# Performance work log

Hardware: AMD Instinct MI355X
Metric: run time of the kernel (lower is better)

## Reference

```python
import jax, jax.numpy as jnp
import numpy as np

B, K, N = 8, 4, 131072
DENSITY = 0.3
NEG_PAD = -1000.0
NEG_IDLE = -1.0e8


def setup_inputs() -> dict:
    rng = np.random.default_rng(0)
    mask_s = rng.random((B, K, N)) < DENSITY  # bool, per-slot variable counts
    mask_a = rng.random((B, K, N)) < DENSITY
    ts = int(mask_s.sum())
    ta = int(mask_a.sum())
    key = jax.random.key(0)
    k1, k2, k3, k4 = jax.random.split(key, 4)
    return {
        "rgb": jax.random.normal(k1, (ts, 3), dtype=jnp.float32),
        "logits_surface": jax.random.normal(k2, (ts, 1), dtype=jnp.float32),
        "logits_air": jax.random.normal(k3, (ta, 1), dtype=jnp.float32),
        "idle_states": (jax.random.uniform(k4, (B, K)) < 0.25).astype(jnp.float32),
        "mask_eval_surface": jnp.asarray(mask_s),
        "mask_eval_air": jnp.asarray(mask_a),
    }


def _expand(mask, values):
    # mask: (B,K,N) bool; values: (total, C) packed in row-major (b,k,n) mask order.
    # Returns (B,K,N,C) where masked positions hold their packed value (others garbage,
    # to be overwritten by the caller's jnp.where). Equivalent to the torch B*K scatter loop.
    m = mask.reshape(-1)
    pos = jnp.cumsum(m.astype(jnp.int32)) - 1  # packed index for each masked slot
    pos = jnp.clip(pos, 0, values.shape[0] - 1)
    return jnp.take(values, pos, axis=0).reshape(mask.shape + (values.shape[-1],))


def reference(rgb, logits_surface, logits_air, idle_states,
              mask_eval_surface, mask_eval_air):
    alive = (1.0 - idle_states)[:, :, None, None]  # (B,K,1,1)
    idle = idle_states[:, :, None, None]
    ms = mask_eval_surface[..., None]  # (B,K,N,1)
    ma = mask_eval_air[..., None]

    rgb_out = jnp.where(ms, _expand(mask_eval_surface, rgb) * alive, 0.0)
    logits_surface_out = jnp.where(
        ms, _expand(mask_eval_surface, logits_surface) * alive + idle * NEG_IDLE, NEG_PAD)
    logits_air_out = jnp.where(
        ma, _expand(mask_eval_air, logits_air) * alive + idle * NEG_IDLE, NEG_PAD)
    return rgb_out, logits_surface_out, logits_air_out
```

## Files before the change

kernel.cpp:

```cpp
#include <hip/hip_runtime.h>
#include <stdint.h>

#define NTOT      4194304LL
#define CHUNK     2048
#define NBLK      2048
#define NEG_PAD   (-1000.0f)
#define NEG_IDLE  (-100000000.0f)
#define CAPS      768
#define CAPA      768

typedef unsigned long long u64;
typedef float float3u __attribute__((ext_vector_type(3), aligned(4)));
typedef float float4a __attribute__((ext_vector_type(4), aligned(16)));
typedef int   int4v   __attribute__((ext_vector_type(4), aligned(16)));

__global__ __launch_bounds__(256, 8) void count_kernel(
    const int* __restrict__ ms, const int* __restrict__ ma,
    unsigned short* __restrict__ cmp, u64* __restrict__ totals)
{
    const int t = threadIdx.x, lane = t & 63, wave = t >> 6;
    const unsigned bid = blockIdx.x;
    const long long base = (long long)bid * CHUNK;

    const int4v* ms4 = (const int4v*)(ms + base);
    const int4v* ma4 = (const int4v*)(ma + base);
    int4v s0 = __builtin_nontemporal_load(ms4 + 2 * t);
    int4v s1 = __builtin_nontemporal_load(ms4 + 2 * t + 1);
    int4v a0 = __builtin_nontemporal_load(ma4 + 2 * t);
    int4v a1 = __builtin_nontemporal_load(ma4 + 2 * t + 1);
    unsigned sbits = (unsigned)(s0[0] != 0)        | ((unsigned)(s0[1] != 0) << 1)
                   | ((unsigned)(s0[2] != 0) << 2) | ((unsigned)(s0[3] != 0) << 3)
                   | ((unsigned)(s1[0] != 0) << 4) | ((unsigned)(s1[1] != 0) << 5)
                   | ((unsigned)(s1[2] != 0) << 6) | ((unsigned)(s1[3] != 0) << 7);
    unsigned abits = (unsigned)(a0[0] != 0)        | ((unsigned)(a0[1] != 0) << 1)
                   | ((unsigned)(a0[2] != 0) << 2) | ((unsigned)(a0[3] != 0) << 3)
                   | ((unsigned)(a1[0] != 0) << 4) | ((unsigned)(a1[1] != 0) << 5)
                   | ((unsigned)(a1[2] != 0) << 6) | ((unsigned)(a1[3] != 0) << 7);

    cmp[bid * 256u + (unsigned)t] = (unsigned short)(sbits | (abits << 8));

    unsigned cnt = __popc(sbits) | (__popc(abits) << 16);
    #pragma unroll
    for (int o = 32; o; o >>= 1) cnt += __shfl_down(cnt, o, 64);
    __shared__ unsigned lds[4];
    if (lane == 0) lds[wave] = cnt;
    __syncthreads();
    if (t == 0) {
        unsigned tot = lds[0] + lds[1] + lds[2] + lds[3];
        totals[bid] = (u64)(tot & 0xffffu) | ((u64)(tot >> 16) << 32);
    }
}

__global__ __launch_bounds__(256, 8) void expand_kernel(
    const float* __restrict__ rgb, const float* __restrict__ lsurf,
    const float* __restrict__ lair, const float* __restrict__ idle,
    const unsigned short* __restrict__ cmp, const u64* __restrict__ totals,
    unsigned rgb_max, unsigned ts_max, unsigned ta_max,
    float* __restrict__ out_rgb, float* __restrict__ out_ls, float* __restrict__ out_la)
{
    __shared__ unsigned wsum[4];
    __shared__ u64 wacc[4];
    __shared__ unsigned packLDS[256];
    __shared__ unsigned prefLDS[256];
    __shared__ float4a rgbSrc4[(CAPS * 3 + 4 + 3) / 4];
    __shared__ float4a lsS4[(CAPS + 4 + 3) / 4];
    __shared__ float4a laS4[(CAPA + 4 + 3) / 4];
    float* const rgbSrc = (float*)rgbSrc4;
    float* const lsS    = (float*)lsS4;
    float* const laS    = (float*)laS4;

    const int t = threadIdx.x, lane = t & 63, wave = t >> 6;
    const unsigned bid = blockIdx.x;
    const long long base = (long long)bid * CHUNK;

    unsigned pk = cmp[bid * 256u + (unsigned)t];
    u64 acc = 0;
    #pragma unroll
    for (int j = 0; j < 8; ++j) {
        unsigned idx = (unsigned)t * 8u + (unsigned)j;
        acc += (idx < bid) ? totals[idx] : 0ULL;
    }
    const float idle_v = idle[(int)(base >> 17)];

    packLDS[t] = pk;
    unsigned cnt = __popc(pk & 0xffu) | (__popc(pk >> 8) << 16);

    unsigned x = cnt;
    #pragma unroll
    for (int o = 1; o < 64; o <<= 1) {
        unsigned y = __shfl_up(x, o, 64);
        if (lane >= o) x += y;
    }
    if (lane == 63) wsum[wave] = x;
    #pragma unroll
    for (int o = 32; o; o >>= 1) acc += __shfl_down(acc, o, 64);
    if (lane == 0) wacc[wave] = acc;
    __syncthreads();
    unsigned pre = (wave > 0 ? wsum[0] : 0u) + (wave > 1 ? wsum[1] : 0u)
                 + (wave > 2 ? wsum[2] : 0u);
    prefLDS[t] = pre + x - cnt;
    u64 basesum = wacc[0] + wacc[1] + wacc[2] + wacc[3];
    const unsigned excS = (unsigned)(basesum & 0xffffffffULL);
    const unsigned excA = (unsigned)(basesum >> 32);
    unsigned totPk = wsum[0] + wsum[1] + wsum[2] + wsum[3];
    const unsigned totS = totPk & 0xffffu;
    const unsigned totA = totPk >> 16;

    const unsigned nS = totS < CAPS ? totS : CAPS;
    const unsigned nA = totA < CAPA ? totA : CAPA;
    const unsigned ofsR = (excS * 3u) & 3u;
    const unsigned ofsS = excS & 3u;
    const unsigned ofsA = excA & 3u;
    {
        const unsigned FR = ofsR + nS * 3u, nvR = FR >> 2, tlR = FR & 3u;
        const unsigned FS = ofsS + nS,      nvS = FS >> 2, tlS = FS & 3u;
        const unsigned FA = ofsA + nA,      nvA = FA >> 2, tlA = FA & 3u;
        const float4a* sR = (const float4a*)(rgb + (excS * 3u - ofsR));
        const float4a* sS = (const float4a*)(lsurf + (excS - ofsS));
        const float4a* sA = (const float4a*)(lair + (excA - ofsA));
        for (unsigned i = t; i < nvR; i += 256u)
            rgbSrc4[i] = __builtin_nontemporal_load(sR + i);
        for (unsigned i = t; i < nvS; i += 256u)
            lsS4[i] = __builtin_nontemporal_load(sS + i);
        for (unsigned i = t; i < nvA; i += 256u)
            laS4[i] = __builtin_nontemporal_load(sA + i);
        if ((unsigned)t < tlR) rgbSrc[4u * nvR + t] = rgb[excS * 3u - ofsR + 4u * nvR + t];
        if ((unsigned)t < tlS) lsS[4u * nvS + t]    = lsurf[excS - ofsS + 4u * nvS + t];
        if ((unsigned)t < tlA) laS[4u * nvA + t]    = lair[excA - ofsA + 4u * nvA + t];
    }
    __syncthreads();

    const float alive     = 1.0f - idle_v;
    const float idle_term = idle_v * NEG_IDLE;
    const int  sub = t >> 3, b = t & 7;
    const unsigned bm = (1u << b) - 1u;
    const int  hp = t >> 1;
    const unsigned nib = (unsigned)(t & 1) * 4u;
    const unsigned nm  = (1u << nib) - 1u;

    #pragma unroll
    for (int g = 0; g < 8; ++g) {
        const int p = (g << 5) + sub;
        unsigned w  = packLDS[p];
        unsigned pv = prefLDS[p];
        const long long e = base + g * 256 + t;
        float vx = 0.f, vy = 0.f, vz = 0.f;
        if ((w >> b) & 1u) {
            unsigned lr = (pv & 0xffffu) + __popc(w & bm);
            if (lr < CAPS) {
                vx = rgbSrc[ofsR + 3u * lr];
                vy = rgbSrc[ofsR + 3u * lr + 1u];
                vz = rgbSrc[ofsR + 3u * lr + 2u];
            } else {
                unsigned pr = excS + lr; pr = pr < rgb_max ? pr : rgb_max;
                float3u v = *(const float3u*)(rgb + 3LL * pr);
                vx = v.x; vy = v.y; vz = v.z;
            }
            vx *= alive; vy *= alive; vz *= alive;
        }
        __builtin_nontemporal_store(vx, out_rgb + 3 * e);
        __builtin_nontemporal_store(vy, out_rgb + 3 * e + 1);
        __builtin_nontemporal_store(vz, out_rgb + 3 * e + 2);
    }

    #pragma unroll
    for (int h = 0; h < 2; ++h) {
        const int p = h * 128 + hp;
        unsigned w  = packLDS[p];
        unsigned pv = prefLDS[p];
        unsigned ws = w & 0xffu, wa = (w >> 8) & 0xffu;
        unsigned baseS = (pv & 0xffffu) + __popc(ws & nm);
        unsigned baseA = (pv >> 16)     + __popc(wa & nm);
        unsigned sb = (ws >> nib) & 0xFu;
        unsigned ab = (wa >> nib) & 0xFu;
        float lsv[4], lav[4];
        #pragma unroll
        for (int j = 0; j < 4; ++j) {
            unsigned mj = (1u << j) - 1u;
            unsigned rs = baseS + __popc(sb & mj);
            float vs = rs < CAPS ? lsS[ofsS + rs]
                     : lsurf[(excS + rs) < ts_max ? (excS + rs) : ts_max];
            lsv[j] = ((sb >> j) & 1u) ? vs * alive + idle_term : NEG_PAD;
            unsigned ra = baseA + __popc(ab & mj);
            float va = ra < CAPA ? laS[ofsA + ra]
                     : lair[(excA + ra) < ta_max ? (excA + ra) : ta_max];
            lav[j] = ((ab >> j) & 1u) ? va * alive + idle_term : NEG_PAD;
        }
        const long long eb = base + h * 1024 + 4 * t;
        float4a vls; vls.x = lsv[0]; vls.y = lsv[1]; vls.z = lsv[2]; vls.w = lsv[3];
        float4a vla; vla.x = lav[0]; vla.y = lav[1]; vla.z = lav[2]; vla.w = lav[3];
        __builtin_nontemporal_store(vls, (float4a*)(out_ls + eb));
        __builtin_nontemporal_store(vla, (float4a*)(out_la + eb));
    }
}

extern "C" void kernel_launch(void* const* d_in, const int* in_sizes, int n_in,
                              void* d_out, int out_size, void* d_ws, size_t ws_size,
                              hipStream_t stream)
{
    const float* rgb   = (const float*)d_in[0];
    const float* lsurf = (const float*)d_in[1];
    const float* lair  = (const float*)d_in[2];
    const float* idle  = (const float*)d_in[3];
    const int*   ms    = (const int*)d_in[4];
    const int*   ma    = (const int*)d_in[5];

    unsigned rgb_max = (unsigned)(in_sizes[0] / 3 - 1);
    unsigned ts_max  = (unsigned)(in_sizes[1] - 1);
    unsigned ta_max  = (unsigned)(in_sizes[2] - 1);

    float* out     = (float*)d_out;
    float* out_rgb = out;
    float* out_ls  = out + NTOT * 3;
    float* out_la  = out_ls + NTOT;

    u64* totals = (u64*)d_ws;
    unsigned short* cmp = (unsigned short*)((char*)d_ws + 16384);

    count_kernel<<<NBLK, 256, 0, stream>>>(ms, ma, cmp, totals);
    expand_kernel<<<NBLK, 256, 0, stream>>>(rgb, lsurf, lair, idle, cmp, totals,
                                            rgb_max, ts_max, ta_max,
                                            out_rgb, out_ls, out_la);
}
```

Measured before the change: 140.7 us.

## Fuse count and expand kernels via cooperative launch with grid sync

Merges the mask-counting pass and the expansion pass into one cooperative kernel that computes per-block counts, publishes totals, then performs a grid-wide sync before computing exclusive offsets and writing outputs. This removes the second kernel launch and the intermediate compressed-mask round trip through global memory. It falls back to the two-kernel path if cooperative launch is unsupported or fails. It requires all 2048 blocks to be co-resident, and the grid barrier adds its own latency.

Result: slower. 320.5 us (+127.7%).

```diff
diff --git a/kernel.cpp b/kernel.cpp
--- a/kernel.cpp
+++ b/kernel.cpp
@@ -1,5 +1,8 @@
 #include <hip/hip_runtime.h>
+#include <hip/hip_cooperative_groups.h>
 #include <stdint.h>
+
+namespace cg = cooperative_groups;
 
 #define NTOT      4194304LL
 #define CHUNK     2048
@@ -14,47 +17,11 @@
 typedef float float4a __attribute__((ext_vector_type(4), aligned(16)));
 typedef int   int4v   __attribute__((ext_vector_type(4), aligned(16)));
 
-__global__ __launch_bounds__(256, 8) void count_kernel(
-    const int* __restrict__ ms, const int* __restrict__ ma,
-    unsigned short* __restrict__ cmp, u64* __restrict__ totals)
-{
-    const int t = threadIdx.x, lane = t & 63, wave = t >> 6;
-    const unsigned bid = blockIdx.x;
-    const long long base = (long long)bid * CHUNK;
-
-    const int4v* ms4 = (const int4v*)(ms + base);
-    const int4v* ma4 = (const int4v*)(ma + base);
-    int4v s0 = __builtin_nontemporal_load(ms4 + 2 * t);
-    int4v s1 = __builtin_nontemporal_load(ms4 + 2 * t + 1);
-    int4v a0 = __builtin_nontemporal_load(ma4 + 2 * t);
-    int4v a1 = __builtin_nontemporal_load(ma4 + 2 * t + 1);
-    unsigned sbits = (unsigned)(s0[0] != 0)        | ((unsigned)(s0[1] != 0) << 1)
-                   | ((unsigned)(s0[2] != 0) << 2) | ((unsigned)(s0[3] != 0) << 3)
-                   | ((unsigned)(s1[0] != 0) << 4) | ((unsigned)(s1[1] != 0) << 5)
-                   | ((unsigned)(s1[2] != 0) << 6) | ((unsigned)(s1[3] != 0) << 7);
-    unsigned abits = (unsigned)(a0[0] != 0)        | ((unsigned)(a0[1] != 0) << 1)
-                   | ((unsigned)(a0[2] != 0) << 2) | ((unsigned)(a0[3] != 0) << 3)
-                   | ((unsigned)(a1[0] != 0) << 4) | ((unsigned)(a1[1] != 0) << 5)
-                   | ((unsigned)(a1[2] != 0) << 6) | ((unsigned)(a1[3] != 0) << 7);
-
-    cmp[bid * 256u + (unsigned)t] = (unsigned short)(sbits | (abits << 8));
-
-    unsigned cnt = __popc(sbits) | (__popc(abits) << 16);
-    #pragma unroll
-    for (int o = 32; o; o >>= 1) cnt += __shfl_down(cnt, o, 64);
-    __shared__ unsigned lds[4];
-    if (lane == 0) lds[wave] = cnt;
-    __syncthreads();
-    if (t == 0) {
-        unsigned tot = lds[0] + lds[1] + lds[2] + lds[3];
-        totals[bid] = (u64)(tot & 0xffffu) | ((u64)(tot >> 16) << 32);
-    }
-}
-
-__global__ __launch_bounds__(256, 8) void expand_kernel(
+__global__ __launch_bounds__(256, 8) void fused_kernel(
     const float* __restrict__ rgb, const float* __restrict__ lsurf,
     const float* __restrict__ lair, const float* __restrict__ idle,
-    const unsigned short* __restrict__ cmp, const u64* __restrict__ totals,
+    const int* __restrict__ ms, const int* __restrict__ ma,
+    u64* __restrict__ totals,
     unsigned rgb_max, unsigned ts_max, unsigned ta_max,
     float* __restrict__ out_rgb, float* __restrict__ out_ls, float* __restrict__ out_la)
 {
@@ -73,36 +40,55 @@
     const unsigned bid = blockIdx.x;
     const long long base = (long long)bid * CHUNK;
 
-    unsigned pk = cmp[bid * 256u + (unsigned)t];
+    const int4v* ms4 = (const int4v*)(ms + base);
+    const int4v* ma4 = (const int4v*)(ma + base);
+    int4v s0 = __builtin_nontemporal_load(ms4 + 2 * t);
+    int4v s1 = __builtin_nontemporal_load(ms4 + 2 * t + 1);
+    int4v a0 = __builtin_nontemporal_load(ma4 + 2 * t);
+    int4v a1 = __builtin_nontemporal_load(ma4 + 2 * t + 1);
+    const float idle_v = idle[(int)(base >> 17)];
+    unsigned sbits = (unsigned)(s0[0] != 0)        | ((unsigned)(s0[1] != 0) << 1)
+                   | ((unsigned)(s0[2] != 0) << 2) | ((unsigned)(s0[3] != 0) << 3)
+                   | ((unsigned)(s1[0] != 0) << 4) | ((unsigned)(s1[1] != 0) << 5)
+                   | ((unsigned)(s1[2] != 0) << 6) | ((unsigned)(s1[3] != 0) << 7);
+    unsigned abits = (unsigned)(a0[0] != 0)        | ((unsigned)(a0[1] != 0) << 1)
+                   | ((unsigned)(a0[2] != 0) << 2) | ((unsigned)(a0[3] != 0) << 3)
+                   | ((unsigned)(a1[0] != 0) << 4) | ((unsigned)(a1[1] != 0) << 5)
+                   | ((unsigned)(a1[2] != 0) << 6) | ((unsigned)(a1[3] != 0) << 7);
+    unsigned pk = sbits | (abits << 8);
+    packLDS[t] = pk;
+    unsigned cnt = __popc(sbits) | (__popc(abits) << 16);
+
+    unsigned x = cnt;
+    #pragma unroll
+    for (int o = 1; o < 64; o <<= 1) {
+        unsigned y = __shfl_up(x, o, 64);
+        if (lane >= o) x += y;
+    }
+    if (lane == 63) wsum[wave] = x;
+    __syncthreads();
+    unsigned pre = (wave > 0 ? wsum[0] : 0u) + (wave > 1 ? wsum[1] : 0u)
+                 + (wave > 2 ? wsum[2] : 0u);
+    prefLDS[t] = pre + x - cnt;
+    unsigned totPk = wsum[0] + wsum[1] + wsum[2] + wsum[3];
+    if (t == 0)
+        totals[bid] = (u64)(totPk & 0xffffu) | ((u64)(totPk >> 16) << 32);
+
+    cg::this_grid().sync();
+
     u64 acc = 0;
     #pragma unroll
     for (int j = 0; j < 8; ++j) {
         unsigned idx = (unsigned)t * 8u + (unsigned)j;
         acc += (idx < bid) ? totals[idx] : 0ULL;
     }
-    const float idle_v = idle[(int)(base >> 17)];
-
-    packLDS[t] = pk;
-    unsigned cnt = __popc(pk & 0xffu) | (__popc(pk >> 8) << 16);
-
-    unsigned x = cnt;
-    #pragma unroll
-    for (int o = 1; o < 64; o <<= 1) {
-        unsigned y = __shfl_up(x, o, 64);
-        if (lane >= o) x += y;
-    }
-    if (lane == 63) wsum[wave] = x;
     #pragma unroll
     for (int o = 32; o; o >>= 1) acc += __shfl_down(acc, o, 64);
     if (lane == 0) wacc[wave] = acc;
     __syncthreads();
-    unsigned pre = (wave > 0 ? wsum[0] : 0u) + (wave > 1 ? wsum[1] : 0u)
-                 + (wave > 2 ? wsum[2] : 0u);
-    prefLDS[t] = pre + x - cnt;
     u64 basesum = wacc[0] + wacc[1] + wacc[2] + wacc[3];
     const unsigned excS = (unsigned)(basesum & 0xffffffffULL);
     const unsigned excA = (unsigned)(basesum >> 32);
-    unsigned totPk = wsum[0] + wsum[1] + wsum[2] + wsum[3];
     const unsigned totS = totPk & 0xffffu;
     const unsigned totA = totPk >> 16;
 
@@ -194,6 +180,186 @@
     }
 }
 
+__global__ __launch_bounds__(256, 8) void count_kernel(
+    const int* __restrict__ ms, const int* __restrict__ ma,
+    unsigned short* __restrict__ cmp, u64* __restrict__ totals)
+{
+    const int t = threadIdx.x, lane = t & 63, wave = t >> 6;
+    const unsigned bid = blockIdx.x;
+    const long long base = (long long)bid * CHUNK;
+
+    const int4v* ms4 = (const int4v*)(ms + base);
+    const int4v* ma4 = (const int4v*)(ma + base);
+    int4v s0 = __builtin_nontemporal_load(ms4 + 2 * t);
+    int4v s1 = __builtin_nontemporal_load(ms4 + 2 * t + 1);
+    int4v a0 = __builtin_nontemporal_load(ma4 + 2 * t);
+    int4v a1 = __builtin_nontemporal_load(ma4 + 2 * t + 1);
+    unsigned sbits = (unsigned)(s0[0] != 0)        | ((unsigned)(s0[1] != 0) << 1)
+                   | ((unsigned)(s0[2] != 0) << 2) | ((unsigned)(s0[3] != 0) << 3)
+                   | ((unsigned)(s1[0] != 0) << 4) | ((unsigned)(s1[1] != 0) << 5)
+                   | ((unsigned)(s1[2] != 0) << 6) | ((unsigned)(s1[3] != 0) << 7);
+    unsigned abits = (unsigned)(a0[0] != 0)        | ((unsigned)(a0[1] != 0) << 1)
+                   | ((unsigned)(a0[2] != 0) << 2) | ((unsigned)(a0[3] != 0) << 3)
+                   | ((unsigned)(a1[0] != 0) << 4) | ((unsigned)(a1[1] != 0) << 5)
+                   | ((unsigned)(a1[2] != 0) << 6) | ((unsigned)(a1[3] != 0) << 7);
+
+    cmp[bid * 256u + (unsigned)t] = (unsigned short)(sbits | (abits << 8));
+
+    unsigned cnt = __popc(sbits) | (__popc(abits) << 16);
+    #pragma unroll
+    for (int o = 32; o; o >>= 1) cnt += __shfl_down(cnt, o, 64);
+    __shared__ unsigned lds[4];
+    if (lane == 0) lds[wave] = cnt;
+    __syncthreads();
+    if (t == 0) {
+        unsigned tot = lds[0] + lds[1] + lds[2] + lds[3];
+        totals[bid] = (u64)(tot & 0xffffu) | ((u64)(tot >> 16) << 32);
+    }
+}
+
+__global__ __launch_bounds__(256, 8) void expand_kernel(
+    const float* __restrict__ rgb, const float* __restrict__ lsurf,
+    const float* __restrict__ lair, const float* __restrict__ idle,
+    const unsigned short* __restrict__ cmp, const u64* __restrict__ totals,
+    unsigned rgb_max, unsigned ts_max, unsigned ta_max,
+    float* __restrict__ out_rgb, float* __restrict__ out_ls, float* __restrict__ out_la)
+{
+    __shared__ unsigned wsum[4];
+    __shared__ u64 wacc[4];
+    __shared__ unsigned packLDS[256];
+    __shared__ unsigned prefLDS[256];
+    __shared__ float4a rgbSrc4[(CAPS * 3 + 4 + 3) / 4];
+    __shared__ float4a lsS4[(CAPS + 4 + 3) / 4];
+    __shared__ float4a laS4[(CAPA + 4 + 3) / 4];
+    float* const rgbSrc = (float*)rgbSrc4;
+    float* const lsS    = (float*)lsS4;
+    float* const laS    = (float*)laS4;
+
+    const int t = threadIdx.x, lane = t & 63, wave = t >> 6;
+    const unsigned bid = blockIdx.x;
+    const long long base = (long long)bid * CHUNK;
+
+    unsigned pk = cmp[bid * 256u + (unsigned)t];
+    u64 acc = 0;
+    #pragma unroll
+    for (int j = 0; j < 8; ++j) {
+        unsigned idx = (unsigned)t * 8u + (unsigned)j;
+        acc += (idx < bid) ? totals[idx] : 0ULL;
+    }
+    const float idle_v = idle[(int)(base >> 17)];
+
+    packLDS[t] = pk;
+    unsigned cnt = __popc(pk & 0xffu) | (__popc(pk >> 8) << 16);
+
+    unsigned x = cnt;
+    #pragma unroll
+    for (int o = 1; o < 64; o <<= 1) {
+        unsigned y = __shfl_up(x, o, 64);
+        if (lane >= o) x += y;
+    }
+    if (lane == 63) wsum[wave] = x;
+    #pragma unroll
+    for (int o = 32; o; o >>= 1) acc += __shfl_down(acc, o, 64);
+    if (lane == 0) wacc[wave] = acc;
+    __syncthreads();
+    unsigned pre = (wave > 0 ? wsum[0] : 0u) + (wave > 1 ? wsum[1] : 0u)
+                 + (wave > 2 ? wsum[2] : 0u);
+    prefLDS[t] = pre + x - cnt;
+    u64 basesum = wacc[0] + wacc[1] + wacc[2] + wacc[3];
+    const unsigned excS = (unsigned)(basesum & 0xffffffffULL);
+    const unsigned excA = (unsigned)(basesum >> 32);
+    unsigned totPk = wsum[0] + wsum[1] + wsum[2] + wsum[3];
+    const unsigned totS = totPk & 0xffffu;
+    const unsigned totA = totPk >> 16;
+
+    const unsigned nS = totS < CAPS ? totS : CAPS;
+    const unsigned nA = totA < CAPA ? totA : CAPA;
+    const unsigned ofsR = (excS * 3u) & 3u;
+    const unsigned ofsS = excS & 3u;
+    const unsigned ofsA = excA & 3u;
+    {
+        const unsigned FR = ofsR + nS * 3u, nvR = FR >> 2, tlR = FR & 3u;
+        const unsigned FS = ofsS + nS,      nvS = FS >> 2, tlS = FS & 3u;
+        const unsigned FA = ofsA + nA,      nvA = FA >> 2, tlA = FA & 3u;
+        const float4a* sR = (const float4a*)(rgb + (excS * 3u - ofsR));
+        const float4a* sS = (const float4a*)(lsurf + (excS - ofsS));
+        const float4a* sA = (const float4a*)(lair + (excA - ofsA));
+        for (unsigned i = t; i < nvR; i += 256u)
+            rgbSrc4[i] = __builtin_nontemporal_load(sR + i);
+        for (unsigned i = t; i < nvS; i += 256u)
+            lsS4[i] = __builtin_nontemporal_load(sS + i);
+        for (unsigned i = t; i < nvA; i += 256u)
+            laS4[i] = __builtin_nontemporal_load(sA + i);
+        if ((unsigned)t < tlR) rgbSrc[4u * nvR + t] = rgb[excS * 3u - ofsR + 4u * nvR + t];
+        if ((unsigned)t < tlS) lsS[4u * nvS + t]    = lsurf[excS - ofsS + 4u * nvS + t];
+        if ((unsigned)t < tlA) laS[4u * nvA + t]    = lair[excA - ofsA + 4u * nvA + t];
+    }
+    __syncthreads();
+
+    const float alive     = 1.0f - idle_v;
+    const float idle_term = idle_v * NEG_IDLE;
+    const int  sub = t >> 3, b = t & 7;
+    const unsigned bm = (1u << b) - 1u;
+    const int  hp = t >> 1;
+    const unsigned nib = (unsigned)(t & 1) * 4u;
+    const unsigned nm  = (1u << nib) - 1u;
+
+    #pragma unroll
+    for (int g = 0; g < 8; ++g) {
+        const int p = (g << 5) + sub;
+        unsigned w  = packLDS[p];
+        unsigned pv = prefLDS[p];
+        const long long e = base + g * 256 + t;
+        float vx = 0.f, vy = 0.f, vz = 0.f;
+        if ((w >> b) & 1u) {
+            unsigned lr = (pv & 0xffffu) + __popc(w & bm);
+            if (lr < CAPS) {
+                vx = rgbSrc[ofsR + 3u * lr];
+                vy = rgbSrc[ofsR + 3u * lr + 1u];
+                vz = rgbSrc[ofsR + 3u * lr + 2u];
+            } else {
+                unsigned pr = excS + lr; pr = pr < rgb_max ? pr : rgb_max;
+                float3u v = *(const float3u*)(rgb + 3LL * pr);
+                vx = v.x; vy = v.y; vz = v.z;
+            }
+            vx *= alive; vy *= alive; vz *= alive;
+        }
+        __builtin_nontemporal_store(vx, out_rgb + 3 * e);
+        __builtin_nontemporal_store(vy, out_rgb + 3 * e + 1);
+        __builtin_nontemporal_store(vz, out_rgb + 3 * e + 2);
+    }
+
+    #pragma unroll
+    for (int h = 0; h < 2; ++h) {
+        const int p = h * 128 + hp;
+        unsigned w  = packLDS[p];
+        unsigned pv = prefLDS[p];
+        unsigned ws = w & 0xffu, wa = (w >> 8) & 0xffu;
+        unsigned baseS = (pv & 0xffffu) + __popc(ws & nm);
+        unsigned baseA = (pv >> 16)     + __popc(wa & nm);
+        unsigned sb = (ws >> nib) & 0xFu;
+        unsigned ab = (wa >> nib) & 0xFu;
+        float lsv[4], lav[4];
+        #pragma unroll
+        for (int j = 0; j < 4; ++j) {
+            unsigned mj = (1u << j) - 1u;
+            unsigned rs = baseS + __popc(sb & mj);
+            float vs = rs < CAPS ? lsS[ofsS + rs]
+                     : lsurf[(excS + rs) < ts_max ? (excS + rs) : ts_max];
+            lsv[j] = ((sb >> j) & 1u) ? vs * alive + idle_term : NEG_PAD;
+            unsigned ra = baseA + __popc(ab & mj);
+            float va = ra < CAPA ? laS[ofsA + ra]
+                     : lair[(excA + ra) < ta_max ? (excA + ra) : ta_max];
+            lav[j] = ((ab >> j) & 1u) ? va * alive + idle_term : NEG_PAD;
+        }
+        const long long eb = base + h * 1024 + 4 * t;
+        float4a vls; vls.x = lsv[0]; vls.y = lsv[1]; vls.z = lsv[2]; vls.w = lsv[3];
+        float4a vla; vla.x = lav[0]; vla.y = lav[1]; vla.z = lav[2]; vla.w = lav[3];
+        __builtin_nontemporal_store(vls, (float4a*)(out_ls + eb));
+        __builtin_nontemporal_store(vla, (float4a*)(out_la + eb));
+    }
+}
+
 extern "C" void kernel_launch(void* const* d_in, const int* in_sizes, int n_in,
                               void* d_out, int out_size, void* d_ws, size_t ws_size,
                               hipStream_t stream)
@@ -217,8 +383,30 @@
     u64* totals = (u64*)d_ws;
     unsigned short* cmp = (unsigned short*)((char*)d_ws + 16384);
 
-    count_kernel<<<NBLK, 256, 0, stream>>>(ms, ma, cmp, totals);
-    expand_kernel<<<NBLK, 256, 0, stream>>>(rgb, lsurf, lair, idle, cmp, totals,
-                                            rgb_max, ts_max, ta_max,
-                                            out_rgb, out_ls, out_la);
+    static int coop_ok = -1;
+    if (coop_ok < 0) {
+        int dev = 0, v = 0;
+        (void)hipGetDevice(&dev);
+        if (hipDeviceGetAttribute(&v, hipDeviceAttributeCooperativeLaunch, dev)
+            != hipSuccess) v = 0;
+        coop_ok = v;
+    }
+
+    hipError_t err = hipErrorUnknown;
+    if (coop_ok) {
+        void* args[] = {
+            (void*)&rgb, (void*)&lsurf, (void*)&lair, (void*)&idle,
+            (void*)&ms, (void*)&ma, (void*)&totals,
+            (void*)&rgb_max, (void*)&ts_max, (void*)&ta_max,
+            (void*)&out_rgb, (void*)&out_ls, (void*)&out_la
+        };
+        err = hipLaunchCooperativeKernel((const void*)fused_kernel,
+                                         dim3(NBLK), dim3(256), args, 0, stream);
+    }
+    if (err != hipSuccess) {
+        count_kernel<<<NBLK, 256, 0, stream>>>(ms, ma, cmp, totals);
+        expand_kernel<<<NBLK, 256, 0, stream>>>(rgb, lsurf, lair, idle, cmp, totals,
+                                                rgb_max, ts_max, ta_max,
+                                                out_rgb, out_ls, out_la);
+    }
 }
```
